# Kernel tuning notes

Hardware: AMD Instinct MI355X
Metric: run time of the kernel (lower is better)

Reference implementation:

```python
import jax, jax.numpy as jnp
import numpy as np

N = 4_000_000   # active fine voxels
C = 32          # feature channels
M = 500_000     # parent (coarse) voxels


def setup_inputs() -> dict:
    key = jax.random.key(0)
    k_feat, k_ids = jax.random.split(key)
    feat = jax.random.normal(k_feat, (N, C), dtype=jnp.float32)
    # child -> parent voxel mapping (sorted, as produced by coordinate-ordered sparse grids)
    segment_ids = jnp.sort(jax.random.randint(k_ids, (N,), 0, M, dtype=jnp.int32))
    return {"feat": feat, "segment_ids": segment_ids, "num_segments": M}


def reference(feat, segment_ids, num_segments):
    # segment-max pooling of fine voxel features into coarse parent cells
    pooled = jax.ops.segment_max(feat, segment_ids, num_segments=num_segments,
                                 indices_are_sorted=True)  # [M, C]
    # empty parents yield -inf; module zeros all inf entries: feat[torch.isinf(feat)] = 0.0
    return jnp.where(jnp.isinf(pooled), jnp.float32(0.0), pooled)
```

## Files before the change

kernel.cpp:

```cpp
#include <hip/hip_runtime.h>
#include <math.h>

#define CCH 32
#define QPR 8
#define CAP 256
#define PCH 33
#define RPT 8
#define CHUNK (32 * RPT)
#define ENC_NEGINF 0x007FFFFFu

typedef float f4 __attribute__((ext_vector_type(4)));

__device__ __forceinline__ unsigned encf(float x) {
    unsigned b = __float_as_uint(x);
    return (b & 0x80000000u) ? ~b : (b | 0x80000000u);
}
__device__ __forceinline__ unsigned decbits(unsigned u) {
    if (u == ENC_NEGINF) return 0u;
    return (u & 0x80000000u) ? (u ^ 0x80000000u) : ~u;
}

__device__ __forceinline__ f4 f4max(f4 a, f4 b) {
    f4 r;
    r.x = fmaxf(a.x, b.x);
    r.y = fmaxf(a.y, b.y);
    r.z = fmaxf(a.z, b.z);
    r.w = fmaxf(a.w, b.w);
    return r;
}

__global__ void bounds_kernel(const int* __restrict__ ids,
                              int* __restrict__ startc,
                              int N, int NB) {
    int j = blockIdx.x * blockDim.x + threadIdx.x;
    if (j > NB) return;
    int target = j * CAP;
    int lo = 0, hi = N;
    while (lo < hi) {
        int mid = (lo + hi) >> 1;
        if (ids[mid] < target) lo = mid + 1;
        else hi = mid;
    }
    startc[j] = lo;
}

__global__ __launch_bounds__(256) void pool_kernel(
    const f4* __restrict__ feat, const int* __restrict__ ids,
    const int* __restrict__ startc, unsigned* __restrict__ out,
    int M) {
    __shared__ unsigned tab[CAP * PCH];
    const int b    = blockIdx.x;
    const int sid0 = b * CAP;
    const int rs   = startc[b];
    const int re   = startc[b + 1];
    const int tid  = threadIdx.x;
    const int q    = tid & (QPR - 1);
    const int rofs = tid >> 3;
    const int c0   = q * 4;

    for (int e = tid; e < CAP * PCH; e += 256) tab[e] = ENC_NEGINF;
    __syncthreads();

    int cbase = rs;
    for (; cbase + CHUNK <= re; cbase += CHUNK) {
        const int r0 = cbase + rofs * RPT;
        f4  v[RPT];
        int s[RPT];
        #pragma unroll
        for (int k = 0; k < RPT; ++k) v[k] = feat[(size_t)(r0 + k) * QPR + q];
        #pragma unroll
        for (int k = 0; k < RPT; ++k) s[k] = ids[r0 + k];

        f4  acc = v[0];
        int cs  = s[0];
        #pragma unroll
        for (int k = 1; k < RPT; ++k) {
            if (s[k] == cs) {
                acc = f4max(acc, v[k]);
            } else {
                unsigned* t = tab + (cs - sid0) * PCH + c0;
                atomicMax(t + 0, encf(acc.x));
                atomicMax(t + 1, encf(acc.y));
                atomicMax(t + 2, encf(acc.z));
                atomicMax(t + 3, encf(acc.w));
                acc = v[k];
                cs  = s[k];
            }
        }
        {
            unsigned* t = tab + (cs - sid0) * PCH + c0;
            atomicMax(t + 0, encf(acc.x));
            atomicMax(t + 1, encf(acc.y));
            atomicMax(t + 2, encf(acc.z));
            atomicMax(t + 3, encf(acc.w));
        }
    }

    if (cbase < re) {
        const int r0 = cbase + rofs * RPT;
        f4  acc;
        int cs = -1;
        #pragma unroll
        for (int k = 0; k < RPT; ++k) {
            int r = r0 + k;
            if (r < re) {
                f4  vv = feat[(size_t)r * QPR + q];
                int ss = ids[r];
                if (ss == cs) {
                    acc = f4max(acc, vv);
                } else {
                    if (cs >= 0) {
                        unsigned* t = tab + (cs - sid0) * PCH + c0;
                        atomicMax(t + 0, encf(acc.x));
                        atomicMax(t + 1, encf(acc.y));
                        atomicMax(t + 2, encf(acc.z));
                        atomicMax(t + 3, encf(acc.w));
                    }
                    acc = vv;
                    cs  = ss;
                }
            }
        }
        if (cs >= 0) {
            unsigned* t = tab + (cs - sid0) * PCH + c0;
            atomicMax(t + 0, encf(acc.x));
            atomicMax(t + 1, encf(acc.y));
            atomicMax(t + 2, encf(acc.z));
            atomicMax(t + 3, encf(acc.w));
        }
    }
    __syncthreads();

    int nsid = M - sid0; if (nsid > CAP) nsid = CAP;
    unsigned* ob = out + (size_t)sid0 * CCH;
    for (int e = tid; e < nsid * CCH; e += 256) {
        unsigned u = tab[(e >> 5) * PCH + (e & 31)];
        ob[e] = decbits(u);
    }
}

extern "C" void kernel_launch(void* const* d_in, const int* in_sizes, int n_in,
                              void* d_out, int out_size, void* d_ws, size_t ws_size,
                              hipStream_t stream) {
    const f4*  feat = (const f4*)d_in[0];
    const int* ids  = (const int*)d_in[1];

    const int N  = in_sizes[0] / CCH;
    const int M  = out_size / CCH;
    const int NB = (M + CAP - 1) / CAP;

    int* startc = (int*)d_ws;

    int gridA = (NB + 1 + 255) / 256;
    bounds_kernel<<<gridA, 256, 0, stream>>>(ids, startc, N, NB);
    pool_kernel<<<NB, 256, 0, stream>>>(feat, ids, startc,
                                        (unsigned*)d_out, M);
}
```

Before: 696.3 us.

## Double segments per block, unpad LDS table, vectorize init/output, unify tail via clamping

```diff
diff --git a/kernel.cpp b/kernel.cpp
--- a/kernel.cpp
+++ b/kernel.cpp
@@ -3,19 +3,21 @@
 
 #define CCH 32
 #define QPR 8
-#define CAP 256
-#define PCH 33
+#define CAP 512
+#define PCH 32
 #define RPT 8
-#define CHUNK (32 * RPT)
+#define CHUNK 256
 #define ENC_NEGINF 0x007FFFFFu
 
 typedef float f4 __attribute__((ext_vector_type(4)));
+typedef unsigned u32;
+typedef u32 u32x4 __attribute__((ext_vector_type(4)));
 
-__device__ __forceinline__ unsigned encf(float x) {
-    unsigned b = __float_as_uint(x);
+__device__ __forceinline__ u32 encf(float x) {
+    u32 b = __float_as_uint(x);
     return (b & 0x80000000u) ? ~b : (b | 0x80000000u);
 }
-__device__ __forceinline__ unsigned decbits(unsigned u) {
+__device__ __forceinline__ u32 decbits(u32 u) {
     if (u == ENC_NEGINF) return 0u;
     return (u & 0x80000000u) ? (u ^ 0x80000000u) : ~u;
 }
@@ -27,6 +29,15 @@
     r.z = fmaxf(a.z, b.z);
     r.w = fmaxf(a.w, b.w);
     return r;
+}
+
+__device__ __forceinline__ void flush(u32* __restrict__ tab, int sidl, int c0,
+                                      f4 acc) {
+    u32* t = tab + sidl * PCH + c0;
+    atomicMax(t + 0, encf(acc.x));
+    atomicMax(t + 1, encf(acc.y));
+    atomicMax(t + 2, encf(acc.z));
+    atomicMax(t + 3, encf(acc.w));
 }
 
 __global__ void bounds_kernel(const int* __restrict__ ids,
@@ -46,9 +57,10 @@
 
 __global__ __launch_bounds__(256) void pool_kernel(
     const f4* __restrict__ feat, const int* __restrict__ ids,
-    const int* __restrict__ startc, unsigned* __restrict__ out,
+    const int* __restrict__ startc, u32* __restrict__ out,
     int M) {
-    __shared__ unsigned tab[CAP * PCH];
+    __shared__ u32 tab[CAP * PCH];
+    u32x4* tab4 = (u32x4*)tab;
     const int b    = blockIdx.x;
     const int sid0 = b * CAP;
     const int rs   = startc[b];
@@ -58,84 +70,54 @@
     const int rofs = tid >> 3;
     const int c0   = q * 4;
 
-    for (int e = tid; e < CAP * PCH; e += 256) tab[e] = ENC_NEGINF;
+    const u32x4 ninf4 = {ENC_NEGINF, ENC_NEGINF, ENC_NEGINF, ENC_NEGINF};
+    for (int i = tid; i < CAP * PCH / 4; i += 256) tab4[i] = ninf4;
     __syncthreads();
 
-    int cbase = rs;
-    for (; cbase + CHUNK <= re; cbase += CHUNK) {
-        const int r0 = cbase + rofs * RPT;
-        f4  v[RPT];
-        int s[RPT];
-        #pragma unroll
-        for (int k = 0; k < RPT; ++k) v[k] = feat[(size_t)(r0 + k) * QPR + q];
-        #pragma unroll
-        for (int k = 0; k < RPT; ++k) s[k] = ids[r0 + k];
+    if (re > rs) {
+        const int rmax = re - 1;
+        for (int cbase = rs; cbase < re; cbase += CHUNK) {
+            const int r0 = cbase + rofs * RPT;
+            f4  v[RPT];
+            int s[RPT];
+            #pragma unroll
+            for (int k = 0; k < RPT; ++k) {
+                int rc = r0 + k; rc = rc < rmax ? rc : rmax;
+                v[k] = feat[(size_t)rc * QPR + q];
+            }
+            #pragma unroll
+            for (int k = 0; k < RPT; ++k) {
+                int rc = r0 + k; rc = rc < rmax ? rc : rmax;
+                s[k] = ids[rc];
+            }
 
-        f4  acc = v[0];
-        int cs  = s[0];
-        #pragma unroll
-        for (int k = 1; k < RPT; ++k) {
-            if (s[k] == cs) {
-                acc = f4max(acc, v[k]);
-            } else {
-                unsigned* t = tab + (cs - sid0) * PCH + c0;
-                atomicMax(t + 0, encf(acc.x));
-                atomicMax(t + 1, encf(acc.y));
-                atomicMax(t + 2, encf(acc.z));
-                atomicMax(t + 3, encf(acc.w));
-                acc = v[k];
-                cs  = s[k];
-            }
-        }
-        {
-            unsigned* t = tab + (cs - sid0) * PCH + c0;
-            atomicMax(t + 0, encf(acc.x));
-            atomicMax(t + 1, encf(acc.y));
-            atomicMax(t + 2, encf(acc.z));
-            atomicMax(t + 3, encf(acc.w));
-        }
-    }
-
-    if (cbase < re) {
-        const int r0 = cbase + rofs * RPT;
-        f4  acc;
-        int cs = -1;
-        #pragma unroll
-        for (int k = 0; k < RPT; ++k) {
-            int r = r0 + k;
-            if (r < re) {
-                f4  vv = feat[(size_t)r * QPR + q];
-                int ss = ids[r];
-                if (ss == cs) {
-                    acc = f4max(acc, vv);
+            f4  acc = v[0];
+            int cs  = s[0];
+            #pragma unroll
+            for (int k = 1; k < RPT; ++k) {
+                if (s[k] == cs) {
+                    acc = f4max(acc, v[k]);
                 } else {
-                    if (cs >= 0) {
-                        unsigned* t = tab + (cs - sid0) * PCH + c0;
-                        atomicMax(t + 0, encf(acc.x));
-                        atomicMax(t + 1, encf(acc.y));
-                        atomicMax(t + 2, encf(acc.z));
-                        atomicMax(t + 3, encf(acc.w));
-                    }
-                    acc = vv;
-                    cs  = ss;
+                    flush(tab, cs - sid0, c0, acc);
+                    acc = v[k];
+                    cs  = s[k];
                 }
             }
-        }
-        if (cs >= 0) {
-            unsigned* t = tab + (cs - sid0) * PCH + c0;
-            atomicMax(t + 0, encf(acc.x));
-            atomicMax(t + 1, encf(acc.y));
-            atomicMax(t + 2, encf(acc.z));
-            atomicMax(t + 3, encf(acc.w));
+            flush(tab, cs - sid0, c0, acc);
         }
     }
     __syncthreads();
 
     int nsid = M - sid0; if (nsid > CAP) nsid = CAP;
-    unsigned* ob = out + (size_t)sid0 * CCH;
-    for (int e = tid; e < nsid * CCH; e += 256) {
-        unsigned u = tab[(e >> 5) * PCH + (e & 31)];
-        ob[e] = decbits(u);
+    u32x4* ob = (u32x4*)(out + (size_t)sid0 * CCH);
+    for (int i = tid; i < nsid * QPR; i += 256) {
+        u32x4 t = tab4[i];
+        u32x4 d;
+        d.x = decbits(t.x);
+        d.y = decbits(t.y);
+        d.z = decbits(t.z);
+        d.w = decbits(t.w);
+        ob[i] = d;
     }
 }
 
@@ -154,5 +136,5 @@
     int gridA = (NB + 1 + 255) / 256;
     bounds_kernel<<<gridA, 256, 0, stream>>>(ids, startc, N, NB);
     pool_kernel<<<NB, 256, 0, stream>>>(feat, ids, startc,
-                                        (unsigned*)d_out, M);
+                                        (u32*)d_out, M);
 }
```

New measurement: 696.6 us. Within noise of the previous version (+0.0%).
